# Optimization experiments

Measured on AMD Instinct MI355X. Metric: run time of the kernel, lower is better.

Reference implementation:

```python
import jax, jax.numpy as jnp
import numpy as np

D_MODEL = 2048
D_HEAD = 128
N_HEADS = D_MODEL // D_HEAD
SEQ_LENS = (512, 768, 384, 384)  # packed varlen sequences, sum = 2048
L_TOTAL = sum(SEQ_LENS)
EPS = 1e-6


def setup_inputs() -> dict:
    key = jax.random.key(0)
    ks = jax.random.split(key, 8)
    x = jax.random.normal(ks[0], (L_TOTAL, D_MODEL), jnp.float32)
    # Flux-style rope table: pairwise-duplicated cos/sin, pe = concat([cos, sin], -1) -> (L, 2*d_head)
    half = D_HEAD // 2
    pos = np.arange(L_TOTAL, dtype=np.float32)[:, None]
    freqs = 1.0 / (10000.0 ** (np.arange(half, dtype=np.float32) / half))  # (half,)
    ang = pos * freqs[None, :]                      # (L, half)
    cos = np.repeat(np.cos(ang), 2, axis=-1)        # (L, d_head), duplicated per pair
    sin = np.repeat(np.sin(ang), 2, axis=-1)
    pe = jnp.asarray(np.concatenate([cos, sin], axis=-1))  # (L, 2*d_head)
    seq_lens = jnp.asarray(SEQ_LENS, dtype=jnp.int32)
    std = 0.02
    qkv_w = std * jax.random.truncated_normal(ks[1], -2.0, 2.0, (3 * D_MODEL, D_MODEL), jnp.float32)
    qkv_b = jnp.zeros((3 * D_MODEL,), jnp.float32)
    q_scale = jnp.ones((D_HEAD,), jnp.float32)
    k_scale = jnp.ones((D_HEAD,), jnp.float32)
    proj_w = std * jax.random.truncated_normal(ks[2], -2.0, 2.0, (D_MODEL, D_MODEL), jnp.float32)
    proj_b = jnp.zeros((D_MODEL,), jnp.float32)
    return {"x": x, "pe": pe, "seq_lens": seq_lens, "qkv_w": qkv_w, "qkv_b": qkv_b,
            "q_scale": q_scale, "k_scale": k_scale, "proj_w": proj_w, "proj_b": proj_b}


def _rms_norm(t, scale):
    tf = t.astype(jnp.float32)
    rrms = jax.lax.rsqrt(jnp.mean(tf * tf, axis=-1, keepdims=True) + EPS)
    return (tf * rrms * scale).astype(t.dtype)


def _apply_rope(t, pe):
    # t: (L, nh, dh); pe: (L, 2*dh) with pairwise-duplicated cos|sin
    L, nh, dh = t.shape
    c = pe[:, None, 0:dh:2]     # (L, 1, dh/2) per-pair cos
    s = pe[:, None, dh::2]      # (L, 1, dh/2) per-pair sin
    tr = t.reshape(L, nh, dh // 2, 2)
    t1, t2 = tr[..., 0], tr[..., 1]
    out = jnp.stack([t1 * c - t2 * s, t1 * s + t2 * c], axis=-1)
    return out.reshape(L, nh, dh)


def reference(x, pe, seq_lens, qkv_w, qkv_b, q_scale, k_scale, proj_w, proj_b):
    L = x.shape[0]
    qkv = x @ qkv_w.T + qkv_b                      # (L, 3*D)
    q, k, v = jnp.split(qkv, 3, axis=-1)
    q = q.reshape(L, N_HEADS, D_HEAD)
    k = k.reshape(L, N_HEADS, D_HEAD)
    v = v.reshape(L, N_HEADS, D_HEAD)
    q = _rms_norm(q, q_scale)
    k = _rms_norm(k, k_scale)
    q = _apply_rope(q, pe)
    k = _apply_rope(k, pe)
    # block-diagonal (packed varlen) attention
    n = seq_lens.shape[0]
    seg = jnp.repeat(jnp.arange(n, dtype=jnp.int32), seq_lens, total_repeat_length=L)  # (L,)
    mask = seg[:, None] == seg[None, :]            # (L, L) block-diagonal
    scale = 1.0 / jnp.sqrt(jnp.float32(D_HEAD))
    scores = jnp.einsum('lhd,mhd->hlm', q, k) * scale  # (nh, L, L)
    scores = jnp.where(mask[None], scores, jnp.finfo(scores.dtype).min)
    p = jax.nn.softmax(scores, axis=-1)
    out = jnp.einsum('hlm,mhd->lhd', p, v)         # (L, nh, dh)
    out = out.reshape(L, D_MODEL)
    return out @ proj_w.T + proj_b
```

## Files before the change

### kernel.cpp

```cpp
#include <hip/hip_runtime.h>

typedef unsigned short ushort_t;
typedef __attribute__((ext_vector_type(4))) float f4;
typedef __attribute__((ext_vector_type(8))) short s8v;
typedef __attribute__((ext_vector_type(8))) __bf16 bf8v;

#define AS1 __attribute__((address_space(1)))
#define AS3 __attribute__((address_space(3)))

__device__ __forceinline__ void async16(void* lds, const void* g) {
    __builtin_amdgcn_global_load_lds((AS1 const void*)g, (AS3 void*)lds, 16, 0, 0);
}

__device__ __forceinline__ f4 mfma16(s8v a, s8v b, f4 c) {
    return __builtin_amdgcn_mfma_f32_16x16x32_bf16(
        __builtin_bit_cast(bf8v, a), __builtin_bit_cast(bf8v, b), c, 0, 0, 0);
}

__device__ __forceinline__ ushort_t f2bf(float f) {
    unsigned int u = __float_as_uint(f);
    u += 0x7fffu + ((u >> 16) & 1u);
    return (ushort_t)(u >> 16);
}
__device__ __forceinline__ float bf2f(ushort_t u) {
    return __uint_as_float(((unsigned int)u) << 16);
}

#define L_TOT   2048
#define DMODEL  2048
#define DHEAD   128
#define NHEADS  16

__global__ __launch_bounds__(256) void cast_all(const float* __restrict__ x,
                                                const float* __restrict__ w1,
                                                ushort_t* __restrict__ xo,
                                                ushort_t* __restrict__ w1o) {
    for (int i = blockIdx.x * 256 + threadIdx.x; i < 4194304; i += 2048 * 256) {
        const float* src; ushort_t* dst; int off;
        if (i < 1048576)      { src = x;  dst = xo;  off = 0; }
        else                  { src = w1; dst = w1o; off = 1048576; }
        int j = i - off;
        float4 v = ((const float4*)src)[j];
        ushort4 o;
        o.x = f2bf(v.x); o.y = f2bf(v.y); o.z = f2bf(v.z); o.w = f2bf(v.w);
        ((ushort4*)dst)[j] = o;
    }
}


template <int P>
__device__ __forceinline__ void cluster(f4 (&acc)[8][4], const s8v (&af)[2][2],
                                        const s8v (&bf)[4][2]) {
    __builtin_amdgcn_s_setprio(1);
#pragma unroll
    for (int mm = 0; mm < 2; mm++)
#pragma unroll
        for (int nn = 0; nn < 4; nn++) {
            acc[2 * P + mm][nn] = mfma16(af[mm][0], bf[nn][0], acc[2 * P + mm][nn]);
            acc[2 * P + mm][nn] = mfma16(af[mm][1], bf[nn][1], acc[2 * P + mm][nn]);
        }
    __builtin_amdgcn_s_setprio(0);
}

#define LDF(base, row, oo) (*(const s8v*)&(base)[(row) * 64 + (oo)])

#define STG(dst, gb, Tt, h)                                                              \
    async16(&(dst)[tid * 8 + (2 * (h)) * 4096],                                          \
            (gb) + (size_t)(Tt) * 64 + (size_t)(128 * (h)) * K);                         \
    async16(&(dst)[tid * 8 + (2 * (h) + 1) * 4096],                                      \
            (gb) + (size_t)(Tt) * 64 + (size_t)(128 * (h) + 64) * K);

#define OPENB()                                                                          \
    __builtin_amdgcn_s_barrier();                                                        \
    asm volatile("s_waitcnt lgkmcnt(0)" ::: "memory");                                   \
    __builtin_amdgcn_sched_barrier(0);

#define TILE(cur, T)                                                                     \
    {                                                                                    \
        const int Tn1 = ((T) + 1 < NT) ? (T) + 1 : NT - 1;                               \
        const int Tn2 = ((T) + 2 < NT) ? (T) + 2 : NT - 1;                               \
        const ushort_t* fA = stA[cur];                                                   \
        const ushort_t* fB = stB[cur];                                                   \
        s8v bfrag[4][2];                                                                 \
        s8v afrag[2][2];                                                                 \
                                                                  \
        bfrag[0][0] = LDF(fB, brow + 0,  o0); bfrag[0][1] = LDF(fB, brow + 0,  o1);      \
        bfrag[1][0] = LDF(fB, brow + 16, o0); bfrag[1][1] = LDF(fB, brow + 16, o1);      \
        bfrag[2][0] = LDF(fB, brow + 32, o0); bfrag[2][1] = LDF(fB, brow + 32, o1);      \
        bfrag[3][0] = LDF(fB, brow + 48, o0); bfrag[3][1] = LDF(fB, brow + 48, o1);      \
        afrag[0][0] = LDF(fA, arow + 0,  o0); afrag[0][1] = LDF(fA, arow + 0,  o1);      \
        afrag[1][0] = LDF(fA, arow + 16, o0); afrag[1][1] = LDF(fA, arow + 16, o1);      \
        STG(stA[(cur) ^ 1], gA, Tn1, 0)                                                  \
        OPENB()                                                                          \
        cluster<0>(acc, afrag, bfrag);                                                   \
        __builtin_amdgcn_s_barrier();                                                    \
                                                                  \
        afrag[0][0] = LDF(fA, arow + 32, o0); afrag[0][1] = LDF(fA, arow + 32, o1);      \
        afrag[1][0] = LDF(fA, arow + 48, o0); afrag[1][1] = LDF(fA, arow + 48, o1);      \
        STG(stA[(cur) ^ 1], gA, Tn1, 1)                                                  \
        OPENB()                                                                          \
        cluster<1>(acc, afrag, bfrag);                                                   \
        __builtin_amdgcn_s_barrier();                                                    \
                                                                  \
        afrag[0][0] = LDF(fA, arow + 64, o0); afrag[0][1] = LDF(fA, arow + 64, o1);      \
        afrag[1][0] = LDF(fA, arow + 80, o0); afrag[1][1] = LDF(fA, arow + 80, o1);      \
        STG(stB[cur], gB, Tn2, 0)                                                        \
        OPENB()                                                                          \
        cluster<2>(acc, afrag, bfrag);                                                   \
        __builtin_amdgcn_s_barrier();                                                    \
                                                                  \
        afrag[0][0] = LDF(fA, arow + 96,  o0); afrag[0][1] = LDF(fA, arow + 96,  o1);    \
        afrag[1][0] = LDF(fA, arow + 112, o0); afrag[1][1] = LDF(fA, arow + 112, o1);    \
        STG(stB[cur], gB, Tn2, 1)                                                        \
        asm volatile("s_waitcnt vmcnt(4)" ::: "memory");                                 \
        __builtin_amdgcn_sched_barrier(0);                                               \
        OPENB()                                                                          \
        cluster<3>(acc, afrag, bfrag);                                                   \
        __builtin_amdgcn_s_barrier();                                                    \
    }

__global__ __launch_bounds__(512, 2) void gemm_qkv256(const ushort_t* __restrict__ A,
                                                      const ushort_t* __restrict__ Bt,
                                                      const float* __restrict__ bias,
                                                      const float* __restrict__ projw,
                                                      ushort_t* __restrict__ projw_bf,
                                                      ushort_t* __restrict__ qk_out,
                                                      ushort_t* __restrict__ vt_out,
                                                      int K) {
    __shared__ alignas(16) ushort_t sA[2][16384];
    __shared__ alignas(16) ushort_t sB[2][16384];

    const int tid  = threadIdx.x;
    const int lane = tid & 63;
    const int wave = tid >> 6;
    const int wm = wave >> 2;
    const int wn = wave & 3;

    const int phys = blockIdx.y * 8 + blockIdx.x;
    const int lid  = (phys & 7) * 32 + (phys >> 3);
    const int xcd  = lid >> 5;
    const int slot = lid & 31;

    if (slot >= 24) {
        const int ci = xcd * 8 + (slot - 24);
#pragma unroll
        for (int it = 0; it < 32; it++) {
            int j = ci * 16384 + it * 512 + tid;
            float4 v = ((const float4*)projw)[j];
            ushort4 o;
            o.x = f2bf(v.x); o.y = f2bf(v.y); o.z = f2bf(v.z); o.w = f2bf(v.w);
            ((ushort4*)projw_bf)[j] = o;
        }
        return;
    }

    const int gid = xcd * 24 + slot;
    const int bxs = gid & 7;
    const int bys = gid >> 3;

    const int bm = bxs * 256;
    const int bn = bys * 256;
    const bool is_v = bys >= 16;
    const int NT = K >> 6;

    const int q15 = lane & 15;
    const int g   = lane >> 4;
    const int l7  = lane & 7;
    const int o0  = ((g    ) ^ l7) * 8;
    const int o1  = ((g + 4) ^ l7) * 8;
    const int arow = wm * 128 + q15;
    const int brow = wn * 64 + q15;

    const int rs  = tid >> 3;
    const int csw = ((tid & 7) ^ (rs & 7)) * 8;
    const ushort_t* Abase = A  + (size_t)(bm + rs) * K + csw;
    const ushort_t* Bbase = Bt + (size_t)(bn + rs) * K + csw;

    ushort_t* stA[2]; ushort_t* stB[2];
    const ushort_t* gA; const ushort_t* gB;
    if (!is_v) { stA[0] = sA[0]; stA[1] = sA[1]; stB[0] = sB[0]; stB[1] = sB[1];
                 gA = Abase; gB = Bbase; }
    else       { stA[0] = sB[0]; stA[1] = sB[1]; stB[0] = sA[0]; stB[1] = sA[1];
                 gA = Bbase; gB = Abase; }

    f4 acc[8][4];
#pragma unroll
    for (int i = 0; i < 8; i++)
#pragma unroll
        for (int j = 0; j < 4; j++) acc[i][j] = (f4){0.f, 0.f, 0.f, 0.f};

    STG(stA[0], gA, 0, 0) STG(stA[0], gA, 0, 1)
    STG(stB[0], gB, 0, 0) STG(stB[0], gB, 0, 1)
    {
        const int T1 = NT > 1 ? 1 : 0;
        STG(stB[1], gB, T1, 0) STG(stB[1], gB, T1, 1)
    }
    asm volatile("s_waitcnt vmcnt(4)" ::: "memory");
    __builtin_amdgcn_sched_barrier(0);
    __builtin_amdgcn_s_barrier();

    for (int T = 0; T < NT; T += 2) {
        TILE(0, T)
        TILE(1, T + 1)
    }

    if (!is_v) {
#pragma unroll
        for (int n = 0; n < 4; n++) {
            int col = bn + wn * 64 + n * 16 + q15;
            float bv = bias[col];
#pragma unroll
            for (int m = 0; m < 8; m++) {
                int r0 = bm + wm * 128 + m * 16 + g * 4;
#pragma unroll
                for (int r = 0; r < 4; r++)
                    qk_out[(size_t)(r0 + r) * 4096 + col] = f2bf(acc[m][n][r] + bv);
            }
        }
    } else {
        const int cb   = (bys - 16) * 256 + wm * 128;
        const int tok0 = bm + wn * 64 + q15;
#pragma unroll
        for (int m = 0; m < 8; m++) {
#pragma unroll
            for (int r = 0; r < 4; r++) {
                int c = cb + m * 16 + g * 4 + r;
                float bv = bias[4096 + c];
#pragma unroll
                for (int n = 0; n < 4; n++)
                    vt_out[(size_t)c * L_TOT + tok0 + n * 16] = f2bf(acc[m][n][r] + bv);
            }
        }
    }
}

__global__ __launch_bounds__(512, 2) void gemm_proj256(const ushort_t* __restrict__ A,
                                                       const ushort_t* __restrict__ Bt,
                                                       float* __restrict__ pAB,
                                                       float* __restrict__ pCD,
                                                       int K) {
    __shared__ alignas(16) ushort_t sA[2][16384];
    __shared__ alignas(16) ushort_t sB[2][16384];

    const int tid  = threadIdx.x;
    const int lane = tid & 63;
    const int wave = tid >> 6;
    const int wm = wave >> 2;
    const int wn = wave & 3;

    const int phys = (blockIdx.z * 8 + blockIdx.y) * 8 + blockIdx.x;
    const int lid  = (phys & 7) * 32 + (phys >> 3);
    const int bxs  = lid & 7;
    const int bys  = (lid >> 3) & 7;
    const int z    = lid >> 6;

    const int bm = bxs * 256;
    const int bn = bys * 256;
    const int NT = K >> 6;
    const int T0 = z * 8;

    const int q15 = lane & 15;
    const int g   = lane >> 4;
    const int l7  = lane & 7;
    const int o0  = ((g    ) ^ l7) * 8;
    const int o1  = ((g + 4) ^ l7) * 8;
    const int arow = wm * 128 + q15;
    const int brow = wn * 64 + q15;

    const int rs  = tid >> 3;
    const int csw = ((tid & 7) ^ (rs & 7)) * 8;
    const ushort_t* gA = A  + (size_t)(bm + rs) * K + csw;
    const ushort_t* gB = Bt + (size_t)(bn + rs) * K + csw;

    ushort_t* stA[2] = { sA[0], sA[1] };
    ushort_t* stB[2] = { sB[0], sB[1] };

    f4 acc[8][4];
#pragma unroll
    for (int i = 0; i < 8; i++)
#pragma unroll
        for (int j = 0; j < 4; j++) acc[i][j] = (f4){0.f, 0.f, 0.f, 0.f};

    STG(stA[0], gA, T0, 0) STG(stA[0], gA, T0, 1)
    STG(stB[0], gB, T0, 0) STG(stB[0], gB, T0, 1)
    STG(stB[1], gB, T0 + 1, 0) STG(stB[1], gB, T0 + 1, 1)
    asm volatile("s_waitcnt vmcnt(4)" ::: "memory");
    __builtin_amdgcn_sched_barrier(0);
    __builtin_amdgcn_s_barrier();

    for (int T = T0; T < T0 + 8; T += 2) {
        TILE(0, T)
        TILE(1, T + 1)
    }

    float* dst = (z < 2 ? pAB + (size_t)z * (L_TOT * DMODEL)
                        : pCD + (size_t)(z - 2) * (L_TOT * DMODEL));
#pragma unroll
    for (int n = 0; n < 4; n++) {
        int col = bn + wn * 64 + n * 16 + q15;
#pragma unroll
        for (int m = 0; m < 8; m++) {
            int r0 = bm + wm * 128 + m * 16 + g * 4;
#pragma unroll
            for (int r = 0; r < 4; r++)
                dst[(size_t)(r0 + r) * DMODEL + col] = acc[m][n][r];
        }
    }
}

__global__ __launch_bounds__(256) void reduce_bias4(const float* __restrict__ pAB,
                                                    const float* __restrict__ pCD,
                                                    const float* __restrict__ bias,
                                                    float* __restrict__ out) {
    int i = blockIdx.x * 256 + threadIdx.x;
    const size_t PL = (size_t)L_TOT * DMODEL / 4;
    f4 a = ((const f4*)pAB)[i];
    f4 b = ((const f4*)pAB)[i + PL];
    f4 c = ((const f4*)pCD)[i];
    f4 d = ((const f4*)pCD)[i + PL];
    f4 bv = ((const f4*)bias)[i & 511];
    ((f4*)out)[i] = (a + b) + (c + d) + bv;
}

__global__ __launch_bounds__(256) void norm_rope(const ushort_t* __restrict__ qk,
                                                 const float* __restrict__ pe,
                                                 const float* __restrict__ q_scale,
                                                 const float* __restrict__ k_scale,
                                                 ushort_t* __restrict__ qh,
                                                 ushort_t* __restrict__ kh) {
    int wid  = blockIdx.x * 4 + (threadIdx.x >> 6);
    int lane = threadIdx.x & 63;
    int l = wid >> 4;
    int h = wid & 15;

    const ushort_t* base = qk + (size_t)l * 4096 + h * DHEAD + 2 * lane;
    ushort2 qu = *(const ushort2*)base;
    ushort2 ku = *(const ushort2*)(base + 2048);
    float qvx = bf2f(qu.x), qvy = bf2f(qu.y);
    float kvx = bf2f(ku.x), kvy = bf2f(ku.y);

    float qss = qvx * qvx + qvy * qvy;
    float kss = kvx * kvx + kvy * kvy;
#pragma unroll
    for (int m = 32; m >= 1; m >>= 1) {
        qss += __shfl_xor(qss, m);
        kss += __shfl_xor(kss, m);
    }
    float qr = rsqrtf(qss * (1.0f / DHEAD) + 1e-6f);
    float kr = rsqrtf(kss * (1.0f / DHEAD) + 1e-6f);

    float c = pe[(size_t)l * 256 + 2 * lane];
    float s = pe[(size_t)l * 256 + 128 + 2 * lane];

    float q1 = qvx * qr * q_scale[2 * lane];
    float q2 = qvy * qr * q_scale[2 * lane + 1];
    float k1 = kvx * kr * k_scale[2 * lane];
    float k2 = kvy * kr * k_scale[2 * lane + 1];

    const float sc = 0.08838834764831845f;
    float qo0 = (q1 * c - q2 * s) * sc;
    float qo1 = (q1 * s + q2 * c) * sc;
    float ko0 = k1 * c - k2 * s;
    float ko1 = k1 * s + k2 * c;

    size_t o = ((size_t)h * L_TOT + l) * DHEAD + 2 * lane;
    ushort2 qp, kp;
    qp.x = f2bf(qo0); qp.y = f2bf(qo1);
    kp.x = f2bf(ko0); kp.y = f2bf(ko1);
    *(ushort2*)(qh + o) = qp;
    *(ushort2*)(kh + o) = kp;
}

__global__ __launch_bounds__(256) void attn_kernel(const ushort_t* __restrict__ qh,
                                                   const ushort_t* __restrict__ kh,
                                                   const ushort_t* __restrict__ vt,
                                                   ushort_t* __restrict__ attn_out) {
    __shared__ alignas(16) ushort_t sK[2][64 * 128];
    __shared__ alignas(16) ushort_t sV[2][128 * 64];
    __shared__ alignas(16) ushort_t sP[4][16 * 64];

    const int phys = blockIdx.y * 32 + blockIdx.x;
    const int lid  = (phys & 7) * 64 + (phys >> 3);
    const int qt = lid & 31;
    const int h  = lid >> 5;

    const int tid = threadIdx.x;
    const int lane = tid & 63;
    const int w = tid >> 6;
    const int qrow0 = qt * 64 + w * 16;

    int q0 = qt * 64;
    int seg_start, seg_end;
    if (q0 < 512)       { seg_start = 0;    seg_end = 512;  }
    else if (q0 < 1280) { seg_start = 512;  seg_end = 1280; }
    else if (q0 < 1664) { seg_start = 1280; seg_end = 1664; }
    else                { seg_start = 1664; seg_end = 2048; }

    const int g = lane >> 4;
    const int q = lane & 15;
    const int qa7 = q & 7;

    const ushort_t* ksrc[4];
    const ushort_t* vsrc[4];
#pragma unroll
    for (int i = 0; i < 4; i++) {
        int p = i * 256 + tid;
        ksrc[i] = kh + ((size_t)h * L_TOT + (p >> 4)) * DHEAD + ((p & 15) ^ ((p >> 4) & 7)) * 8;
        vsrc[i] = vt + ((size_t)h * DHEAD + (p >> 3)) * L_TOT + ((p & 7) ^ ((p >> 3) & 7)) * 8;
    }

    s8v qf[4];
    {
        const ushort_t* qbase = qh + ((size_t)h * L_TOT + qrow0 + q) * DHEAD;
#pragma unroll
        for (int kd = 0; kd < 4; kd++) qf[kd] = *(const s8v*)(qbase + kd * 32 + g * 8);
    }

    f4 o[8];
#pragma unroll
    for (int j = 0; j < 8; j++) o[j] = (f4){0.f, 0.f, 0.f, 0.f};
    float lsum[4] = {0.f, 0.f, 0.f, 0.f};

#pragma unroll
    for (int i = 0; i < 4; i++) {
        int p = i * 256 + tid;
        async16(&sK[0][p * 8], ksrc[i] + (size_t)seg_start * DHEAD);
        async16(&sV[0][p * 8], vsrc[i] + seg_start);
    }

    int cur = 0;
    for (int kt = seg_start; kt < seg_end; kt += 64) {
        if (kt + 64 < seg_end) {
#pragma unroll
            for (int i = 0; i < 4; i++) {
                int p = i * 256 + tid;
                async16(&sK[cur ^ 1][p * 8], ksrc[i] + (size_t)(kt + 64) * DHEAD);
                async16(&sV[cur ^ 1][p * 8], vsrc[i] + (kt + 64));
            }
            asm volatile("s_waitcnt vmcnt(8)" ::: "memory");
        } else {
            asm volatile("s_waitcnt vmcnt(0)" ::: "memory");
        }
        __builtin_amdgcn_sched_barrier(0);
        __syncthreads();

        const ushort_t* Kc = sK[cur];
        const ushort_t* Vc = sV[cur];

        f4 S[4];
        __builtin_amdgcn_s_setprio(1);
#pragma unroll
        for (int tj = 0; tj < 4; tj++) {
            f4 st = (f4){0.f, 0.f, 0.f, 0.f};
#pragma unroll
            for (int kd = 0; kd < 4; kd++) {
                s8v bfrag = *(const s8v*)&Kc[(tj * 16 + q) * 128 + (((kd * 4 + g) ^ qa7) * 8)];
                st = mfma16(qf[kd], bfrag, st);
            }
            S[tj] = st;
        }
        __builtin_amdgcn_s_setprio(0);

#pragma unroll
        for (int tj = 0; tj < 4; tj++)
#pragma unroll
            for (int r = 0; r < 4; r++) {
                float p = __expf(S[tj][r]);
                S[tj][r] = p;
                lsum[r] += p;
            }

#pragma unroll
        for (int tj = 0; tj < 4; tj++) {
            int cg = tj * 2 + (q >> 3);
#pragma unroll
            for (int r = 0; r < 4; r++) {
                int prow = g * 4 + r;
                sP[w][prow * 64 + ((cg ^ (prow & 7)) * 8) + qa7] = f2bf(S[tj][r]);
            }
        }
        asm volatile("s_waitcnt lgkmcnt(0)" ::: "memory");

        __builtin_amdgcn_s_setprio(1);
#pragma unroll
        for (int ks = 0; ks < 2; ks++) {
            s8v pf = *(const s8v*)&sP[w][q * 64 + (((ks * 4 + g) ^ qa7) * 8)];
#pragma unroll
            for (int j = 0; j < 8; j++) {
                s8v vf = *(const s8v*)&Vc[(j * 16 + q) * 64 + (((ks * 4 + g) ^ qa7) * 8)];
                o[j] = mfma16(pf, vf, o[j]);
            }
        }
        __builtin_amdgcn_s_setprio(0);
        __syncthreads();
        cur ^= 1;
    }

#pragma unroll
    for (int r = 0; r < 4; r++) {
        float rs = lsum[r];
        rs += __shfl_xor(rs, 1);
        rs += __shfl_xor(rs, 2);
        rs += __shfl_xor(rs, 4);
        rs += __shfl_xor(rs, 8);
        int row = qrow0 + g * 4 + r;
        float inv = 1.0f / rs;
#pragma unroll
        for (int j = 0; j < 8; j++) {
            attn_out[(size_t)row * DMODEL + h * DHEAD + j * 16 + q] = f2bf(o[j][r] * inv);
        }
    }
}

extern "C" void kernel_launch(void* const* d_in, const int* in_sizes, int n_in,
                              void* d_out, int out_size, void* d_ws, size_t ws_size,
                              hipStream_t stream) {
    const float* x       = (const float*)d_in[0];
    const float* pe      = (const float*)d_in[1];
    const float* qkv_w   = (const float*)d_in[3];
    const float* qkv_b   = (const float*)d_in[4];
    const float* q_scale = (const float*)d_in[5];
    const float* k_scale = (const float*)d_in[6];
    const float* proj_w  = (const float*)d_in[7];
    const float* proj_b  = (const float*)d_in[8];
    float* out = (float*)d_out;

    char* ws = (char*)d_ws;
    const size_t MB = 1024 * 1024;
    ushort_t* x_bf     = (ushort_t*)(ws + 0);
    ushort_t* wqkv_bf  = (ushort_t*)(ws + 8 * MB);
    ushort_t* wproj_bf = (ushort_t*)(ws + 32 * MB);
    ushort_t* qk_bf    = (ushort_t*)(ws + 40 * MB);
    ushort_t* qh       = (ushort_t*)(ws + 57 * MB);
    ushort_t* kh       = (ushort_t*)(ws + 65 * MB);
    ushort_t* vt       = (ushort_t*)(ws + 73 * MB);
    ushort_t* attn_b   = (ushort_t*)(ws + 81 * MB);
    float*    pAB      = (float*)   (ws + 0);
    float*    pCD      = (float*)   (ws + 40 * MB);

    cast_all<<<2048, 256, 0, stream>>>(x, qkv_w, x_bf, wqkv_bf);

    gemm_qkv256<<<dim3(8, 32), 512, 0, stream>>>(x_bf, wqkv_bf, qkv_b,
                                                 proj_w, wproj_bf,
                                                 qk_bf, vt, 2048);

    norm_rope<<<8192, 256, 0, stream>>>(qk_bf, pe, q_scale, k_scale, qh, kh);

    attn_kernel<<<dim3(32, 16), 256, 0, stream>>>(qh, kh, vt, attn_b);

    gemm_proj256<<<dim3(8, 8, 4), 512, 0, stream>>>(attn_b, wproj_bf, pAB, pCD, 2048);
    reduce_bias4<<<4096, 256, 0, stream>>>(pAB, pCD, proj_b, out);
}
```

Baseline: 257.0 us.

## Use 256x128 tiles with 2-way split-K for output projection GEMM

The projection GEMM moves from 256x256 tiles with 4-way split-K to 256x128 tiles with 2-way split-K, keeping 256 workgroups but giving each one 16 K-tiles instead of 8. A new TILEP pipeline and clusterP MFMA cluster handle the narrower B tile. The reduction kernel now sums two fp32 partials instead of four, which cuts partial-buffer write and read traffic. In exchange, each workgroup reuses its operands less and runs a longer serial K loop.

Result: faster. 250.1 us (-2.7%).

```diff
diff --git a/kernel.cpp b/kernel.cpp
--- a/kernel.cpp
+++ b/kernel.cpp
@@ -62,6 +62,20 @@
     __builtin_amdgcn_s_setprio(0);
 }
 
+template <int P>
+__device__ __forceinline__ void clusterP(f4 (&acc)[8][2], const s8v (&af)[2][2],
+                                         const s8v (&bf)[2][2]) {
+    __builtin_amdgcn_s_setprio(1);
+#pragma unroll
+    for (int mm = 0; mm < 2; mm++)
+#pragma unroll
+        for (int nn = 0; nn < 2; nn++) {
+            acc[2 * P + mm][nn] = mfma16(af[mm][0], bf[nn][0], acc[2 * P + mm][nn]);
+            acc[2 * P + mm][nn] = mfma16(af[mm][1], bf[nn][1], acc[2 * P + mm][nn]);
+        }
+    __builtin_amdgcn_s_setprio(0);
+}
+
 #define LDF(base, row, oo) (*(const s8v*)&(base)[(row) * 64 + (oo)])
 
 #define STG(dst, gb, Tt, h)                                                              \
@@ -116,6 +130,47 @@
         __builtin_amdgcn_sched_barrier(0);                                               \
         OPENB()                                                                          \
         cluster<3>(acc, afrag, bfrag);                                                   \
+        __builtin_amdgcn_s_barrier();                                                    \
+    }
+
+#define TILEP(cur, T)                                                                    \
+    {                                                                                    \
+        const int Tn1 = ((T) + 1 < NT) ? (T) + 1 : NT - 1;                               \
+        const int Tn2 = ((T) + 2 < NT) ? (T) + 2 : NT - 1;                               \
+        const ushort_t* fA = stA[cur];                                                   \
+        const ushort_t* fB = stB[cur];                                                   \
+        s8v bfrag[2][2];                                                                 \
+        s8v afrag[2][2];                                                                 \
+                                                                  \
+        bfrag[0][0] = LDF(fB, brow + 0,  o0); bfrag[0][1] = LDF(fB, brow + 0,  o1);      \
+        bfrag[1][0] = LDF(fB, brow + 16, o0); bfrag[1][1] = LDF(fB, brow + 16, o1);      \
+        afrag[0][0] = LDF(fA, arow + 0,  o0); afrag[0][1] = LDF(fA, arow + 0,  o1);      \
+        afrag[1][0] = LDF(fA, arow + 16, o0); afrag[1][1] = LDF(fA, arow + 16, o1);      \
+        STG(stA[(cur) ^ 1], gA, Tn1, 0)                                                  \
+        OPENB()                                                                          \
+        clusterP<0>(acc, afrag, bfrag);                                                  \
+        __builtin_amdgcn_s_barrier();                                                    \
+                                                                  \
+        afrag[0][0] = LDF(fA, arow + 32, o0); afrag[0][1] = LDF(fA, arow + 32, o1);      \
+        afrag[1][0] = LDF(fA, arow + 48, o0); afrag[1][1] = LDF(fA, arow + 48, o1);      \
+        STG(stA[(cur) ^ 1], gA, Tn1, 1)                                                  \
+        OPENB()                                                                          \
+        clusterP<1>(acc, afrag, bfrag);                                                  \
+        __builtin_amdgcn_s_barrier();                                                    \
+                                                                  \
+        afrag[0][0] = LDF(fA, arow + 64, o0); afrag[0][1] = LDF(fA, arow + 64, o1);      \
+        afrag[1][0] = LDF(fA, arow + 80, o0); afrag[1][1] = LDF(fA, arow + 80, o1);      \
+        STG(stB[cur], gB, Tn2, 0)                                                        \
+        OPENB()                                                                          \
+        clusterP<2>(acc, afrag, bfrag);                                                  \
+        __builtin_amdgcn_s_barrier();                                                    \
+                                                                  \
+        afrag[0][0] = LDF(fA, arow + 96,  o0); afrag[0][1] = LDF(fA, arow + 96,  o1);    \
+        afrag[1][0] = LDF(fA, arow + 112, o0); afrag[1][1] = LDF(fA, arow + 112, o1);    \
+        asm volatile("s_waitcnt vmcnt(2)" ::: "memory");                                 \
+        __builtin_amdgcn_sched_barrier(0);                                               \
+        OPENB()                                                                          \
+        clusterP<3>(acc, afrag, bfrag);                                                  \
         __builtin_amdgcn_s_barrier();                                                    \
     }
 
@@ -236,11 +291,10 @@
 
 __global__ __launch_bounds__(512, 2) void gemm_proj256(const ushort_t* __restrict__ A,
                                                        const ushort_t* __restrict__ Bt,
-                                                       float* __restrict__ pAB,
-                                                       float* __restrict__ pCD,
+                                                       float* __restrict__ pP,
                                                        int K) {
-    __shared__ alignas(16) ushort_t sA[2][16384];
-    __shared__ alignas(16) ushort_t sB[2][16384];
+    __shared__ alignas(16) ushort_t sAp[2][16384];
+    __shared__ alignas(16) ushort_t sBp[2][8192];
 
     const int tid  = threadIdx.x;
     const int lane = tid & 63;
@@ -248,16 +302,16 @@
     const int wm = wave >> 2;
     const int wn = wave & 3;
 
-    const int phys = (blockIdx.z * 8 + blockIdx.y) * 8 + blockIdx.x;
+    const int phys = (blockIdx.z * 16 + blockIdx.y) * 8 + blockIdx.x;
     const int lid  = (phys & 7) * 32 + (phys >> 3);
     const int bxs  = lid & 7;
-    const int bys  = (lid >> 3) & 7;
-    const int z    = lid >> 6;
+    const int bys  = (lid >> 3) & 15;
+    const int z    = lid >> 7;
 
     const int bm = bxs * 256;
-    const int bn = bys * 256;
+    const int bn = bys * 128;
     const int NT = K >> 6;
-    const int T0 = z * 8;
+    const int T0 = z * 16;
 
     const int q15 = lane & 15;
     const int g   = lane >> 4;
@@ -265,39 +319,38 @@
     const int o0  = ((g    ) ^ l7) * 8;
     const int o1  = ((g + 4) ^ l7) * 8;
     const int arow = wm * 128 + q15;
-    const int brow = wn * 64 + q15;
+    const int brow = wn * 32 + q15;
 
     const int rs  = tid >> 3;
     const int csw = ((tid & 7) ^ (rs & 7)) * 8;
     const ushort_t* gA = A  + (size_t)(bm + rs) * K + csw;
     const ushort_t* gB = Bt + (size_t)(bn + rs) * K + csw;
 
-    ushort_t* stA[2] = { sA[0], sA[1] };
-    ushort_t* stB[2] = { sB[0], sB[1] };
-
-    f4 acc[8][4];
+    ushort_t* stA[2] = { sAp[0], sAp[1] };
+    ushort_t* stB[2] = { sBp[0], sBp[1] };
+
+    f4 acc[8][2];
 #pragma unroll
     for (int i = 0; i < 8; i++)
 #pragma unroll
-        for (int j = 0; j < 4; j++) acc[i][j] = (f4){0.f, 0.f, 0.f, 0.f};
+        for (int j = 0; j < 2; j++) acc[i][j] = (f4){0.f, 0.f, 0.f, 0.f};
 
     STG(stA[0], gA, T0, 0) STG(stA[0], gA, T0, 1)
-    STG(stB[0], gB, T0, 0) STG(stB[0], gB, T0, 1)
-    STG(stB[1], gB, T0 + 1, 0) STG(stB[1], gB, T0 + 1, 1)
-    asm volatile("s_waitcnt vmcnt(4)" ::: "memory");
+    STG(stB[0], gB, T0, 0)
+    STG(stB[1], gB, T0 + 1, 0)
+    asm volatile("s_waitcnt vmcnt(2)" ::: "memory");
     __builtin_amdgcn_sched_barrier(0);
     __builtin_amdgcn_s_barrier();
 
-    for (int T = T0; T < T0 + 8; T += 2) {
-        TILE(0, T)
-        TILE(1, T + 1)
-    }
-
-    float* dst = (z < 2 ? pAB + (size_t)z * (L_TOT * DMODEL)
-                        : pCD + (size_t)(z - 2) * (L_TOT * DMODEL));
-#pragma unroll
-    for (int n = 0; n < 4; n++) {
-        int col = bn + wn * 64 + n * 16 + q15;
+    for (int T = T0; T < T0 + 16; T += 2) {
+        TILEP(0, T)
+        TILEP(1, T + 1)
+    }
+
+    float* dst = pP + (size_t)z * (L_TOT * DMODEL);
+#pragma unroll
+    for (int n = 0; n < 2; n++) {
+        int col = bn + wn * 32 + n * 16 + q15;
 #pragma unroll
         for (int m = 0; m < 8; m++) {
             int r0 = bm + wm * 128 + m * 16 + g * 4;
@@ -308,18 +361,15 @@
     }
 }
 
-__global__ __launch_bounds__(256) void reduce_bias4(const float* __restrict__ pAB,
-                                                    const float* __restrict__ pCD,
+__global__ __launch_bounds__(256) void reduce_bias2(const float* __restrict__ pP,
                                                     const float* __restrict__ bias,
                                                     float* __restrict__ out) {
     int i = blockIdx.x * 256 + threadIdx.x;
     const size_t PL = (size_t)L_TOT * DMODEL / 4;
-    f4 a = ((const f4*)pAB)[i];
-    f4 b = ((const f4*)pAB)[i + PL];
-    f4 c = ((const f4*)pCD)[i];
-    f4 d = ((const f4*)pCD)[i + PL];
+    f4 a = ((const f4*)pP)[i];
+    f4 b = ((const f4*)pP)[i + PL];
     f4 bv = ((const f4*)bias)[i & 511];
-    ((f4*)out)[i] = (a + b) + (c + d) + bv;
+    ((f4*)out)[i] = a + b + bv;
 }
 
 __global__ __launch_bounds__(256) void norm_rope(const ushort_t* __restrict__ qk,
@@ -535,8 +585,7 @@
     ushort_t* kh       = (ushort_t*)(ws + 65 * MB);
     ushort_t* vt       = (ushort_t*)(ws + 73 * MB);
     ushort_t* attn_b   = (ushort_t*)(ws + 81 * MB);
-    float*    pAB      = (float*)   (ws + 0);
-    float*    pCD      = (float*)   (ws + 40 * MB);
+    float*    pP       = (float*)   (ws + 40 * MB);
 
     cast_all<<<2048, 256, 0, stream>>>(x, qkv_w, x_bf, wqkv_bf);
 
@@ -548,6 +597,6 @@
 
     attn_kernel<<<dim3(32, 16), 256, 0, stream>>>(qh, kh, vt, attn_b);
 
-    gemm_proj256<<<dim3(8, 8, 4), 512, 0, stream>>>(attn_b, wproj_bf, pAB, pCD, 2048);
-    reduce_bias4<<<4096, 256, 0, stream>>>(pAB, pCD, proj_b, out);
-}
+    gemm_proj256<<<dim3(8, 16, 2), 512, 0, stream>>>(attn_b, wproj_bf, pP, 2048);
+    reduce_bias2<<<4096, 256, 0, stream>>>(pP, proj_b, out);
+}
```
